# Optimization experiments

Measured on AMD Instinct MI355X. Metric: run time of the kernel, lower is better.

The kernel has to match this reference:

```python
import jax, jax.numpy as jnp
import numpy as np

MD = 4       # max displacement per level (md=[4,...] in VCN)
WSIZE = 3    # truncation window half-size in flow_reg


def _corrf(ref, tar, md=MD):
    """VCN.corrf: per-channel shifted-product 4D cost volume + leaky_relu.
    cost[b,c,i,j,y,x] = leaky_relu(ref[b,c,y,x] * tar[b,c,y+(j-md), x+(i-md)], 0.1)
    (zero outside valid region, matching the torch zero-filled buffer)."""
    B, C, H, W = ref.shape
    U = 2 * md + 1
    tar_pad = jnp.pad(tar, ((0, 0), (0, 0), (md, md), (md, md)))
    # dim 2 ordered as i*U + j (i = x-shift index, j = y-shift index)
    shifts = jnp.stack([tar_pad[:, :, j:j + H, i:i + W]
                        for i in range(U) for j in range(U)], axis=2)
    cost = jax.nn.leaky_relu(ref[:, :, None] * shifts, 0.1)
    return cost.reshape(B, C, U, U, H, W)


def _flow_reg(x, md=MD, wsize=WSIZE):
    """flow_reg with ent=True: argmax -> 7x7 box mask over (u,v) (the MaxPool3d on a
    one-hot scatter is exactly a Chebyshev-box around the argmax) -> masked softmax
    over u*v -> soft-argmax flow + local/global entropies."""
    B, U, V, H, W = x.shape
    idx = jnp.argmax(x.reshape(B, U * V, H, W), axis=1)         # (B,H,W)
    ub, vb = idx // V, idx % V
    uu = jnp.arange(U)[None, :, None, None, None]
    vv = jnp.arange(V)[None, None, :, None, None]
    mask = (jnp.abs(uu - ub[:, None, None]) <= wsize) & \
           (jnp.abs(vv - vb[:, None, None]) <= wsize)           # (B,U,V,H,W)
    neg_inf = jnp.array(-jnp.inf, x.dtype)
    p = jax.nn.softmax(jnp.where(mask, x, neg_inf).reshape(B, U * V, H, W),
                       axis=1).reshape(B, U, V, H, W)
    fx = (jnp.arange(U) - md).astype(x.dtype)[None, :, None, None, None]
    fy = (jnp.arange(V) - md).astype(x.dtype)[None, None, :, None, None]
    outx = jnp.sum(p * fx, axis=(1, 2))[:, None]                # (B,1,H,W)
    outy = jnp.sum(p * fy, axis=(1, 2))[:, None]
    def _ent(q):
        return (-q * jnp.log(jnp.clip(q, 1e-9, 1 - 1e-9))).sum(axis=(1, 2))[:, None]
    local_ent = _ent(p) / np.log((2 * wsize + 1) ** 2).astype(np.float32)
    pg = jax.nn.softmax(x.reshape(B, U * V, H, W), axis=1).reshape(B, U, V, H, W)
    global_ent = _ent(pg) / np.log(U * V).astype(np.float32)
    return jnp.concatenate([outx, outy], 1), jnp.concatenate([local_ent, global_ent], 1)


def _warp(x, flo):
    """grid_sample-based backward warp (bilinear, zero padding, align_corners=True)
    plus the in-bounds mask, exactly as VCN's warp()."""
    B, C, H, W = x.shape
    px = jnp.arange(W, dtype=flo.dtype)[None, None, :] + flo[:, 0]   # (B,H,W)
    py = jnp.arange(H, dtype=flo.dtype)[None, :, None] + flo[:, 1]
    inb = (jnp.abs(2.0 * px / max(W - 1, 1) - 1.0) < 1) & \
          (jnp.abs(2.0 * py / max(H - 1, 1) - 1.0) < 1)
    x0 = jnp.floor(px); y0 = jnp.floor(py)
    wx = px - x0; wy = py - y0
    x0i = x0.astype(jnp.int32); y0i = y0.astype(jnp.int32)
    flat = x.reshape(B, C, H * W)
    def tap(yi, xi, wgt):
        valid = (xi >= 0) & (xi < W) & (yi >= 0) & (yi < H)
        lin = jnp.clip(yi, 0, H - 1) * W + jnp.clip(xi, 0, W - 1)
        v = jax.vmap(lambda img, l: img[:, l])(flat, lin)            # (B,C,H,W)
        return v * (wgt * valid.astype(x.dtype))[:, None]
    out = (tap(y0i,     x0i,     (1 - wx) * (1 - wy)) +
           tap(y0i,     x0i + 1, wx * (1 - wy)) +
           tap(y0i + 1, x0i,     (1 - wx) * wy) +
           tap(y0i + 1, x0i + 1, wx * wy))
    return out * inb.astype(x.dtype)[:, None], inb


def setup_inputs() -> dict:
    key = jax.random.key(0)
    k1, k2, k3 = jax.random.split(key, 3)
    B, C, H, W, F = 2, 128, 64, 64, 16
    ref = jax.random.normal(k1, (B, C, H, W), jnp.float32) * 0.5
    tar = jax.random.normal(k2, (B, C, H, W), jnp.float32) * 0.5
    pw = jax.random.normal(k3, (F, C), jnp.float32) / np.sqrt(C).astype(np.float32)
    return {"ref_feat": ref, "tar_feat": tar, "proj_w": pw}


def reference(ref_feat, tar_feat, proj_w):
    B, C, H, W = ref_feat.shape
    F_ = proj_w.shape[0]
    U = 2 * MD + 1
    cost = _corrf(ref_feat, tar_feat)                       # (B,C,U,U,H,W)
    # 1x1 channel contraction of the 4D cost volume (butterfly4D input proj)
    cvol = jnp.einsum('bcuvhw,fc->bfuvhw', cost, proj_w)    # (B,F,U,U,H,W)
    flow_h, ent_h = _flow_reg(cvol.reshape(B * F_, U, U, H, W))
    flow = flow_h.reshape(B, F_, 2, H, W)[:, 0]             # first hypothesis
    warped, _ = _warp(tar_feat, flow)
    return jnp.concatenate([flow_h, ent_h], axis=1), warped
```

## Files before the change

kernel.cpp:

```cpp
#include <hip/hip_runtime.h>
#include <math.h>

#define B_ 2
#define C_ 128
#define H_ 64
#define W_ 64
#define F_ 16
#define U_ 9
#define MD_ 4
#define HW_ (H_*W_)
#define BF_ (B_*F_)

typedef float f32x4 __attribute__((ext_vector_type(4)));
typedef float f32x2 __attribute__((ext_vector_type(2)));
typedef _Float16 f16x2 __attribute__((ext_vector_type(2)));
typedef _Float16 f16x4 __attribute__((ext_vector_type(4)));
typedef _Float16 f16x8 __attribute__((ext_vector_type(8)));

#define XSCALE   64.0f
#define WSCALE   256.0f
#define UNSCALE  (1.0f / 16384.0f)

#define TB0  0
#define TB1  7344
#define TSTR 34
#define REFO 14688
#define MXo  0
#define IXo  3168
#define SBo  6336
#define FX_  12672
#define FY_  12688
#define LDSZ 16800

static __device__ __forceinline__ f16x8 cat4(f16x2 a, f16x2 b, f16x2 c, f16x2 d) {
    f16x4 ab = __builtin_shufflevector(a, b, 0, 1, 2, 3);
    f16x4 cd = __builtin_shufflevector(c, d, 0, 1, 2, 3);
    return __builtin_shufflevector(ab, cd, 0, 1, 2, 3, 4, 5, 6, 7);
}

static __device__ __forceinline__ void split2(f32x2 p, f16x2& hi, f16x2& lo) {
    hi = __builtin_bit_cast(f16x2, __builtin_amdgcn_cvt_pkrtz(p.x, p.y));
    f32x2 hf; hf.x = (float)hi.x; hf.y = (float)hi.y;
    f32x2 l = p - hf;
    lo = __builtin_bit_cast(f16x2, __builtin_amdgcn_cvt_pkrtz(l.x, l.y));
}

__global__ __launch_bounds__(768, 2)
void fused_kernel(const float* __restrict__ ref,
                  const float* __restrict__ tar,
                  const float* __restrict__ pw,
                  float* __restrict__ out0,
                  float* __restrict__ warped) {
    const int t    = threadIdx.x;
    const int lane = t & 63;
    const int wid  = t >> 6;
    const int ml   = lane & 15;
    const int grp  = lane >> 4;

    const int n0 = blockIdx.x;
    const int L  = (n0 & 7) * 64 + (n0 >> 3);
    const int b  = L >> 8;
    const int y  = (L >> 2) & 63;
    const int x0 = (L & 3) * 16;

    const bool big = (wid < 9);
    const int start = __builtin_amdgcn_readfirstlane(
        big ? wid * 7 : 63 + (wid - 9) * 6);

    __shared__ float lds[LDSZ];

    const float* refB = ref + ((size_t)b * C_) * HW_ + y * W_ + x0;
    const float* tarB = tar + ((size_t)b * C_) * HW_;

    int off[7], uA[7], vA[7];
    #pragma unroll
    for (int i = 0; i < 7; ++i) {
        int uv = start + i;
        int uu = uv / 9;
        uA[i] = uu; vA[i] = uv - uu * 9;
        off[i] = (vA[i] * 24 + uu) * TSTR;
    }
    const int mlg = ml * TSTR + grp * 8;

    const int seg   = t >> 1;
    const int chalf = (t & 1) * 16;
    const bool sact = (seg < 216);
    const int sr   = seg / 24;
    const int scol = seg - sr * 24;
    const int ysr  = y + sr - 4;
    const int xg   = x0 - 4 + scol;
    const bool sok = sact && ((unsigned)ysr < 64u) && ((unsigned)xg < 64u);
    const int ysc  = ysr < 0 ? 0 : (ysr > 63 ? 63 : ysr);
    const int xgc  = xg  < 0 ? 0 : (xg  > 63 ? 63 : xg);
    const float* tS = tarB + (size_t)chalf * HW_ + ysc * W_ + xgc;

    auto STAGE = [&](int kcv, int bufbase, bool zfill) {
        if (sok) {
            float* dst = lds + bufbase + seg * TSTR + chalf;
            const float* g = tS + (size_t)(kcv * 32) * HW_;
            #pragma unroll
            for (int c0 = 0; c0 < 16; ++c0) dst[c0] = g[(size_t)c0 * HW_];
        } else if (sact && zfill) {
            float* dst = lds + bufbase + seg * TSTR + chalf;
            #pragma unroll
            for (int c0 = 0; c0 < 16; ++c0) dst[c0] = 0.f;
        }
    };

    f32x4 acc[7];
    #pragma unroll
    for (int i = 0; i < 7; ++i) acc[i] = f32x4{0.f, 0.f, 0.f, 0.f};

    #pragma unroll
    for (int it = 0; it < 3; ++it) {
        int idx = it * 768 + t;
        if (idx < 2048) {
            int c = idx >> 4, px = idx & 15;
            lds[REFO + px * 132 + c] = refB[(size_t)c * HW_ + px] * XSCALE;
        }
    }
    STAGE(0, TB0, true);
    __syncthreads();

    #pragma unroll
    for (int kc = 0; kc < 4; ++kc) {
        const int tb = (kc & 1) ? TB1 : TB0;
        if (kc == 0) STAGE(1, TB1, true);
        else if (kc == 1) STAGE(2, TB0, false);
        else if (kc == 2) STAGE(3, TB1, false);

        f32x4 wa = *(const f32x4*)(pw + ml * C_ + kc * 32 + grp * 8);
        f32x4 wb = *(const f32x4*)(pw + ml * C_ + kc * 32 + grp * 8 + 4);
        f16x2 wh[4], wl[4];
        {
            f32x2 p;
            p.x = wa.x * WSCALE; p.y = wa.y * WSCALE; split2(p, wh[0], wl[0]);
            p.x = wa.z * WSCALE; p.y = wa.w * WSCALE; split2(p, wh[1], wl[1]);
            p.x = wb.x * WSCALE; p.y = wb.y * WSCALE; split2(p, wh[2], wl[2]);
            p.x = wb.z * WSCALE; p.y = wb.w * WSCALE; split2(p, wh[3], wl[3]);
        }
        f16x8 whi = cat4(wh[0], wh[1], wh[2], wh[3]);
        f16x8 wlo = cat4(wl[0], wl[1], wl[2], wl[3]);

        f32x4 rva = *(const f32x4*)(lds + REFO + ml * 132 + kc * 32 + grp * 8);
        f32x4 rvb = *(const f32x4*)(lds + REFO + ml * 132 + kc * 32 + grp * 8 + 4);
        f32x2 rv2[4];
        rv2[0].x = rva.x; rv2[0].y = rva.y;
        rv2[1].x = rva.z; rv2[1].y = rva.w;
        rv2[2].x = rvb.x; rv2[2].y = rvb.y;
        rv2[3].x = rvb.z; rv2[3].y = rvb.w;

#define UVBODY(i) {                                                           \
        const float* tp = lds + tb + off[i] + mlg;                            \
        f16x2 xh4[4], xl4[4];                                                 \
        _Pragma("unroll")                                                     \
        for (int jp = 0; jp < 4; ++jp) {                                      \
            f32x2 tj = *(const f32x2*)(tp + 2 * jp);                          \
            f32x2 p  = rv2[jp] * tj;                                          \
            f32x2 p1 = p * 0.1f;                                              \
            p = __builtin_elementwise_max(p, p1);                             \
            split2(p, xh4[jp], xl4[jp]);                                      \
        }                                                                     \
        f16x8 xhi = cat4(xh4[0], xh4[1], xh4[2], xh4[3]);                     \
        f16x8 xlo = cat4(xl4[0], xl4[1], xl4[2], xl4[3]);                     \
        acc[i] = __builtin_amdgcn_mfma_f32_16x16x32_f16(whi, xhi, acc[i], 0, 0, 0); \
        acc[i] = __builtin_amdgcn_mfma_f32_16x16x32_f16(wlo, xhi, acc[i], 0, 0, 0); \
        acc[i] = __builtin_amdgcn_mfma_f32_16x16x32_f16(whi, xlo, acc[i], 0, 0, 0); }

        #pragma unroll
        for (int i = 0; i < 6; ++i) UVBODY(i);
        if (big) UVBODY(6);

        __syncthreads();
    }

    #pragma unroll
    for (int i = 0; i < 7; ++i) acc[i] = acc[i] * UNSCALE;

    f32x4 mx = acc[0];
    f32x4 bix = f32x4{(float)start, (float)start, (float)start, (float)start};
    #pragma unroll
    for (int i = 1; i < 6; ++i)
        #pragma unroll
        for (int r = 0; r < 4; ++r)
            if (acc[i][r] > mx[r]) { mx[r] = acc[i][r]; bix[r] = (float)(start + i); }
    if (big) {
        #pragma unroll
        for (int r = 0; r < 4; ++r)
            if (acc[6][r] > mx[r]) { mx[r] = acc[6][r]; bix[r] = (float)(start + 6); }
    }
    *(f32x4*)(lds + MXo + (wid * 4 + grp) * 66 + ml * 4) = mx;
    *(f32x4*)(lds + IXo + (wid * 4 + grp) * 66 + ml * 4) = bix;
    __syncthreads();

    f32x4 gm = *(const f32x4*)(lds + MXo + grp * 66 + ml * 4);
    f32x4 gb = *(const f32x4*)(lds + IXo + grp * 66 + ml * 4);
    #pragma unroll
    for (int ch = 1; ch < 12; ++ch) {
        f32x4 cm = *(const f32x4*)(lds + MXo + (ch * 4 + grp) * 66 + ml * 4);
        f32x4 cb = *(const f32x4*)(lds + IXo + (ch * 4 + grp) * 66 + ml * 4);
        #pragma unroll
        for (int r = 0; r < 4; ++r)
            if (cm[r] > gm[r]) { gm[r] = cm[r]; gb[r] = cb[r]; }
    }
    int ub[4], vb[4];
    #pragma unroll
    for (int r = 0; r < 4; ++r) {
        int bI = (int)gb[r];
        ub[r] = bI / 9; vb[r] = bI - 9 * ub[r];
    }

    float S[4]  = {0.f,0.f,0.f,0.f}, Aa[4] = {0.f,0.f,0.f,0.f};
    float Sx[4] = {0.f,0.f,0.f,0.f}, Sy[4] = {0.f,0.f,0.f,0.f};
    float gS[4] = {0.f,0.f,0.f,0.f}, gA[4] = {0.f,0.f,0.f,0.f};
#define PHB(i) {                                                              \
        _Pragma("unroll")                                                     \
        for (int r = 0; r < 4; ++r) {                                         \
            float d = acc[i][r] - gm[r];                                      \
            float z = __expf(d);                                              \
            gS[r] += z; gA[r] = fmaf(z, d, gA[r]);                            \
            int duc = uA[i] - ub[r], dvc = vA[i] - vb[r];                     \
            bool msk = (duc <= 3) && (duc >= -3) && (dvc <= 3) && (dvc >= -3);\
            float zm = msk ? z : 0.f, dm = msk ? d : 0.f;                     \
            S[r] += zm; Aa[r] = fmaf(zm, dm, Aa[r]);                          \
            Sx[r] = fmaf(zm, (float)(uA[i] - MD_), Sx[r]);                    \
            Sy[r] = fmaf(zm, (float)(vA[i] - MD_), Sy[r]);                    \
        } }
    #pragma unroll
    for (int i = 0; i < 6; ++i) PHB(i);
    if (big) PHB(6);

    float rq[6];
    const int cml = t & 15, cgrp = (t >> 4) & 3;
#define ROUND(QA, QB, RA, RB) {                                               \
        *(f32x4*)(lds + SBo + ((0 * 12 + wid) * 4 + grp) * 66 + ml * 4) =     \
            f32x4{QA[0], QA[1], QA[2], QA[3]};                                \
        *(f32x4*)(lds + SBo + ((1 * 12 + wid) * 4 + grp) * 66 + ml * 4) =     \
            f32x4{QB[0], QB[1], QB[2], QB[3]};                                \
        __syncthreads();                                                      \
        if (t < 64) {                                                         \
            f32x4 sa = *(const f32x4*)(lds + SBo + ((0) * 4 + cgrp) * 66 + cml * 4); \
            f32x4 sb = *(const f32x4*)(lds + SBo + ((12) * 4 + cgrp) * 66 + cml * 4); \
            _Pragma("unroll")                                                 \
            for (int ch = 1; ch < 12; ++ch) {                                 \
                sa += *(const f32x4*)(lds + SBo + ((ch) * 4 + cgrp) * 66 + cml * 4);      \
                sb += *(const f32x4*)(lds + SBo + ((12 + ch) * 4 + cgrp) * 66 + cml * 4); \
            }                                                                 \
            RA = sa; RB = sb;                                                 \
        }                                                                     \
        __syncthreads(); }
    f32x4 r0v, r1v, r2v, r3v, r4v, r5v;
    ROUND(S,  Aa, r0v, r1v)
    ROUND(Sx, Sy, r2v, r3v)
    ROUND(gS, gA, r4v, r5v)

    if (t < 64) {
        #pragma unroll
        for (int r = 0; r < 4; ++r) {
            float invS = 1.f / r0v[r];
            float outx = r2v[r] * invS;
            float outy = r3v[r] * invS;
            float lent = (logf(r0v[r]) - r1v[r] * invS) * (1.0f / logf(49.0f));
            float gent = (logf(r4v[r]) - r5v[r] / r4v[r]) * (1.0f / logf(81.0f));
            float* op = out0 + ((size_t)(b * F_ + cgrp * 4 + r) * 4) * HW_
                      + y * W_ + x0 + cml;
            op[0 * HW_] = outx;
            op[1 * HW_] = outy;
            op[2 * HW_] = lent;
            op[3 * HW_] = gent;
            if (r == 0 && cgrp == 0) { lds[FX_ + cml] = outx; lds[FY_ + cml] = outy; }
        }
    }
    __syncthreads();

    if (t < 512) {
        const int pxi = t & 15;
        const int xw  = x0 + pxi;
        float fx = lds[FX_ + pxi], fy = lds[FY_ + pxi];
        float pxw = (float)xw + fx;
        float pyw = (float)y  + fy;
        bool inb = (fabsf(2.0f * pxw / 63.0f - 1.0f) < 1.0f) &&
                   (fabsf(2.0f * pyw / 63.0f - 1.0f) < 1.0f);
        float xf = floorf(pxw), yf = floorf(pyw);
        float wx = pxw - xf, wy = pyw - yf;
        int x0i = (int)xf, y0i = (int)yf;
        auto offn = [&](int yi, int xi, float wgt, float& mw) -> int {
            bool v = ((unsigned)xi < (unsigned)W_) && ((unsigned)yi < (unsigned)H_);
            int xc = xi < 0 ? 0 : (xi > W_ - 1 ? W_ - 1 : xi);
            int yc = yi < 0 ? 0 : (yi > H_ - 1 ? H_ - 1 : yi);
            mw = v ? wgt : 0.f;
            return yc * W_ + xc;
        };
        float m00, m01, m10, m11;
        int o00 = offn(y0i,     x0i,     (1.f - wx) * (1.f - wy), m00);
        int o01 = offn(y0i,     x0i + 1, wx * (1.f - wy),         m01);
        int o10 = offn(y0i + 1, x0i,     (1.f - wx) * wy,         m10);
        int o11 = offn(y0i + 1, x0i + 1, wx * wy,                 m11);
        #pragma unroll
        for (int it = 0; it < 4; ++it) {
            int c = (t >> 4) + 32 * it;
            const float* img = tarB + (size_t)c * HW_;
            float a = img[o00] * m00 + img[o01] * m01
                    + img[o10] * m10 + img[o11] * m11;
            warped[((size_t)(b * C_ + c)) * HW_ + y * W_ + xw] = inb ? a : 0.f;
        }
    }
}

extern "C" void kernel_launch(void* const* d_in, const int* in_sizes, int n_in,
                              void* d_out, int out_size, void* d_ws, size_t ws_size,
                              hipStream_t stream) {
    const float* ref = (const float*)d_in[0];
    const float* tar = (const float*)d_in[1];
    const float* pw  = (const float*)d_in[2];
    float* out0 = (float*)d_out;
    float* out1 = out0 + (size_t)BF_ * 4 * HW_;
    (void)d_ws; (void)ws_size;

    fused_kernel<<<512, 768, 0, stream>>>(ref, tar, pw, out0, out1);
}
```

Measured before the change: 104.5 us.

## Shrink blocks to 8 waves with single LDS buffer for higher occupancy

Reworks the kernel from 12 waves handling 6-7 displacement pairs each to 8 waves handling 10-11 each, and launches 512 threads per block with a 3-blocks-per-CU bound. The tar staging goes from double-buffered to a single buffer with an odd 33-float stride, and the reduction buffer now overlaps the max/index scratch, cutting LDS use so more blocks fit per CU. The reduction rounds are merged from three two-value rounds into two three-value rounds to save barriers. In exchange, staging is no longer overlapped with MFMA work and needs an extra barrier per chunk, and each wave holds more accumulators, which raises register pressure.

```diff
diff --git a/kernel.cpp b/kernel.cpp
--- a/kernel.cpp
+++ b/kernel.cpp
@@ -21,16 +21,14 @@
 #define WSCALE   256.0f
 #define UNSCALE  (1.0f / 16384.0f)
 
-#define TB0  0
-#define TB1  7344
-#define TSTR 34
-#define REFO 14688
+#define TSTR 33
+#define REFO 7128
 #define MXo  0
-#define IXo  3168
-#define SBo  6336
-#define FX_  12672
-#define FY_  12688
-#define LDSZ 16800
+#define IXo  2112
+#define SBo  0
+#define FX_  6400
+#define FY_  6416
+#define LDSZ 9240
 
 static __device__ __forceinline__ f16x8 cat4(f16x2 a, f16x2 b, f16x2 c, f16x2 d) {
     f16x4 ab = __builtin_shufflevector(a, b, 0, 1, 2, 3);
@@ -45,7 +43,7 @@
     lo = __builtin_bit_cast(f16x2, __builtin_amdgcn_cvt_pkrtz(l.x, l.y));
 }
 
-__global__ __launch_bounds__(768, 2)
+__global__ __launch_bounds__(512, 3)
 void fused_kernel(const float* __restrict__ ref,
                   const float* __restrict__ tar,
                   const float* __restrict__ pw,
@@ -63,18 +61,16 @@
     const int y  = (L >> 2) & 63;
     const int x0 = (L & 3) * 16;
 
-    const bool big = (wid < 9);
-    const int start = __builtin_amdgcn_readfirstlane(
-        big ? wid * 7 : 63 + (wid - 9) * 6);
+    const int start = __builtin_amdgcn_readfirstlane(wid ? (1 + wid * 10) : 0);
 
     __shared__ float lds[LDSZ];
 
     const float* refB = ref + ((size_t)b * C_) * HW_ + y * W_ + x0;
     const float* tarB = tar + ((size_t)b * C_) * HW_;
 
-    int off[7], uA[7], vA[7];
-    #pragma unroll
-    for (int i = 0; i < 7; ++i) {
+    int off[11], uA[11], vA[11];
+    #pragma unroll
+    for (int i = 0; i < 11; ++i) {
         int uv = start + i;
         int uu = uv / 9;
         uA[i] = uu; vA[i] = uv - uu * 9;
@@ -94,41 +90,34 @@
     const int xgc  = xg  < 0 ? 0 : (xg  > 63 ? 63 : xg);
     const float* tS = tarB + (size_t)chalf * HW_ + ysc * W_ + xgc;
 
-    auto STAGE = [&](int kcv, int bufbase, bool zfill) {
+    auto STAGE = [&](int kcv, bool zfill) {
         if (sok) {
-            float* dst = lds + bufbase + seg * TSTR + chalf;
+            float* dst = lds + seg * TSTR + chalf;
             const float* g = tS + (size_t)(kcv * 32) * HW_;
             #pragma unroll
             for (int c0 = 0; c0 < 16; ++c0) dst[c0] = g[(size_t)c0 * HW_];
         } else if (sact && zfill) {
-            float* dst = lds + bufbase + seg * TSTR + chalf;
+            float* dst = lds + seg * TSTR + chalf;
             #pragma unroll
             for (int c0 = 0; c0 < 16; ++c0) dst[c0] = 0.f;
         }
     };
 
-    f32x4 acc[7];
-    #pragma unroll
-    for (int i = 0; i < 7; ++i) acc[i] = f32x4{0.f, 0.f, 0.f, 0.f};
-
-    #pragma unroll
-    for (int it = 0; it < 3; ++it) {
-        int idx = it * 768 + t;
-        if (idx < 2048) {
-            int c = idx >> 4, px = idx & 15;
-            lds[REFO + px * 132 + c] = refB[(size_t)c * HW_ + px] * XSCALE;
-        }
-    }
-    STAGE(0, TB0, true);
+    f32x4 acc[11];
+    #pragma unroll
+    for (int i = 0; i < 11; ++i) acc[i] = f32x4{0.f, 0.f, 0.f, 0.f};
+
+    #pragma unroll
+    for (int it = 0; it < 4; ++it) {
+        int idx = it * 512 + t;
+        int c = idx >> 4, px = idx & 15;
+        lds[REFO + px * 132 + c] = refB[(size_t)c * HW_ + px] * XSCALE;
+    }
+    STAGE(0, true);
     __syncthreads();
 
     #pragma unroll
     for (int kc = 0; kc < 4; ++kc) {
-        const int tb = (kc & 1) ? TB1 : TB0;
-        if (kc == 0) STAGE(1, TB1, true);
-        else if (kc == 1) STAGE(2, TB0, false);
-        else if (kc == 2) STAGE(3, TB1, false);
-
         f32x4 wa = *(const f32x4*)(pw + ml * C_ + kc * 32 + grp * 8);
         f32x4 wb = *(const f32x4*)(pw + ml * C_ + kc * 32 + grp * 8 + 4);
         f16x2 wh[4], wl[4];
@@ -151,11 +140,11 @@
         rv2[3].x = rvb.z; rv2[3].y = rvb.w;
 
 #define UVBODY(i) {                                                           \
-        const float* tp = lds + tb + off[i] + mlg;                            \
+        const float* tp = lds + off[i] + mlg;                                 \
         f16x2 xh4[4], xl4[4];                                                 \
         _Pragma("unroll")                                                     \
         for (int jp = 0; jp < 4; ++jp) {                                      \
-            f32x2 tj = *(const f32x2*)(tp + 2 * jp);                          \
+            f32x2 tj; tj.x = tp[2 * jp]; tj.y = tp[2 * jp + 1];               \
             f32x2 p  = rv2[jp] * tj;                                          \
             f32x2 p1 = p * 0.1f;                                              \
             p = __builtin_elementwise_max(p, p1);                             \
@@ -168,26 +157,30 @@
         acc[i] = __builtin_amdgcn_mfma_f32_16x16x32_f16(whi, xlo, acc[i], 0, 0, 0); }
 
         #pragma unroll
-        for (int i = 0; i < 6; ++i) UVBODY(i);
-        if (big) UVBODY(6);
+        for (int i = 0; i < 10; ++i) UVBODY(i);
+        if (wid == 0) UVBODY(10);
 
         __syncthreads();
-    }
-
-    #pragma unroll
-    for (int i = 0; i < 7; ++i) acc[i] = acc[i] * UNSCALE;
+        if (kc < 3) {
+            STAGE(kc + 1, false);
+            __syncthreads();
+        }
+    }
+
+    #pragma unroll
+    for (int i = 0; i < 11; ++i) acc[i] = acc[i] * UNSCALE;
 
     f32x4 mx = acc[0];
     f32x4 bix = f32x4{(float)start, (float)start, (float)start, (float)start};
     #pragma unroll
-    for (int i = 1; i < 6; ++i)
+    for (int i = 1; i < 10; ++i)
         #pragma unroll
         for (int r = 0; r < 4; ++r)
             if (acc[i][r] > mx[r]) { mx[r] = acc[i][r]; bix[r] = (float)(start + i); }
-    if (big) {
+    if (wid == 0) {
         #pragma unroll
         for (int r = 0; r < 4; ++r)
-            if (acc[6][r] > mx[r]) { mx[r] = acc[6][r]; bix[r] = (float)(start + 6); }
+            if (acc[10][r] > mx[r]) { mx[r] = acc[10][r]; bix[r] = 10.f; }
     }
     *(f32x4*)(lds + MXo + (wid * 4 + grp) * 66 + ml * 4) = mx;
     *(f32x4*)(lds + IXo + (wid * 4 + grp) * 66 + ml * 4) = bix;
@@ -196,7 +189,7 @@
     f32x4 gm = *(const f32x4*)(lds + MXo + grp * 66 + ml * 4);
     f32x4 gb = *(const f32x4*)(lds + IXo + grp * 66 + ml * 4);
     #pragma unroll
-    for (int ch = 1; ch < 12; ++ch) {
+    for (int ch = 1; ch < 8; ++ch) {
         f32x4 cm = *(const f32x4*)(lds + MXo + (ch * 4 + grp) * 66 + ml * 4);
         f32x4 cb = *(const f32x4*)(lds + IXo + (ch * 4 + grp) * 66 + ml * 4);
         #pragma unroll
@@ -227,32 +220,35 @@
             Sy[r] = fmaf(zm, (float)(vA[i] - MD_), Sy[r]);                    \
         } }
     #pragma unroll
-    for (int i = 0; i < 6; ++i) PHB(i);
-    if (big) PHB(6);
-
-    float rq[6];
+    for (int i = 0; i < 10; ++i) PHB(i);
+    if (wid == 0) PHB(10);
+    __syncthreads();
+
     const int cml = t & 15, cgrp = (t >> 4) & 3;
-#define ROUND(QA, QB, RA, RB) {                                               \
-        *(f32x4*)(lds + SBo + ((0 * 12 + wid) * 4 + grp) * 66 + ml * 4) =     \
+#define ROUND3(QA, QB, QC, RA, RB, RC) {                                      \
+        *(f32x4*)(lds + SBo + ((0 * 8 + wid) * 4 + grp) * 66 + ml * 4) =      \
             f32x4{QA[0], QA[1], QA[2], QA[3]};                                \
-        *(f32x4*)(lds + SBo + ((1 * 12 + wid) * 4 + grp) * 66 + ml * 4) =     \
+        *(f32x4*)(lds + SBo + ((1 * 8 + wid) * 4 + grp) * 66 + ml * 4) =      \
             f32x4{QB[0], QB[1], QB[2], QB[3]};                                \
+        *(f32x4*)(lds + SBo + ((2 * 8 + wid) * 4 + grp) * 66 + ml * 4) =      \
+            f32x4{QC[0], QC[1], QC[2], QC[3]};                                \
         __syncthreads();                                                      \
         if (t < 64) {                                                         \
-            f32x4 sa = *(const f32x4*)(lds + SBo + ((0) * 4 + cgrp) * 66 + cml * 4); \
-            f32x4 sb = *(const f32x4*)(lds + SBo + ((12) * 4 + cgrp) * 66 + cml * 4); \
+            f32x4 sa = *(const f32x4*)(lds + SBo + ((0 * 8) * 4 + cgrp) * 66 + cml * 4); \
+            f32x4 sb = *(const f32x4*)(lds + SBo + ((1 * 8) * 4 + cgrp) * 66 + cml * 4); \
+            f32x4 sc = *(const f32x4*)(lds + SBo + ((2 * 8) * 4 + cgrp) * 66 + cml * 4); \
             _Pragma("unroll")                                                 \
-            for (int ch = 1; ch < 12; ++ch) {                                 \
-                sa += *(const f32x4*)(lds + SBo + ((ch) * 4 + cgrp) * 66 + cml * 4);      \
-                sb += *(const f32x4*)(lds + SBo + ((12 + ch) * 4 + cgrp) * 66 + cml * 4); \
+            for (int ch = 1; ch < 8; ++ch) {                                  \
+                sa += *(const f32x4*)(lds + SBo + ((0 * 8 + ch) * 4 + cgrp) * 66 + cml * 4); \
+                sb += *(const f32x4*)(lds + SBo + ((1 * 8 + ch) * 4 + cgrp) * 66 + cml * 4); \
+                sc += *(const f32x4*)(lds + SBo + ((2 * 8 + ch) * 4 + cgrp) * 66 + cml * 4); \
             }                                                                 \
-            RA = sa; RB = sb;                                                 \
+            RA = sa; RB = sb; RC = sc;                                        \
         }                                                                     \
         __syncthreads(); }
     f32x4 r0v, r1v, r2v, r3v, r4v, r5v;
-    ROUND(S,  Aa, r0v, r1v)
-    ROUND(Sx, Sy, r2v, r3v)
-    ROUND(gS, gA, r4v, r5v)
+    ROUND3(S,  Aa, Sx, r0v, r1v, r2v)
+    ROUND3(Sy, gS, gA, r3v, r4v, r5v)
 
     if (t < 64) {
         #pragma unroll
@@ -273,7 +269,7 @@
     }
     __syncthreads();
 
-    if (t < 512) {
+    {
         const int pxi = t & 15;
         const int xw  = x0 + pxi;
         float fx = lds[FX_ + pxi], fy = lds[FY_ + pxi];
@@ -317,5 +313,5 @@
     float* out1 = out0 + (size_t)BF_ * 4 * HW_;
     (void)d_ws; (void)ws_size;
 
-    fused_kernel<<<512, 768, 0, stream>>>(ref, tar, pw, out0, out1);
+    fused_kernel<<<512, 512, 0, stream>>>(ref, tar, pw, out0, out1);
 }
```

Measured after the change: 96.87 us. 7.3% less time.
